# Kernel optimization log

Measured on AMD Instinct MI355X. Metric: run time of the kernel, lower is better.

## Reference

```python
import jax, jax.numpy as jnp
import numpy as np

B, Q, DIN, DOUT = 1, 1024, 4096, 4096
H, G, HD = 32, 8, 128          # heads, kv groups, head_dim; group_size = H // G
PREV = 3072                     # cached KV length
MAXPOS = 4096                   # rope table length (>= PREV + Q)
START = PREV


def _rope_tables(max_pos, head_dim):
    half = head_dim // 2
    inv_freq = 1.0 / (10000.0 ** (jnp.arange(half, dtype=jnp.float32) / half))
    ang = jnp.arange(max_pos, dtype=jnp.float32)[:, None] * inv_freq[None, :]
    ang = jnp.concatenate([ang, ang], axis=-1)  # [max_pos, head_dim]
    return jnp.cos(ang), jnp.sin(ang)


def apply_rope(x, cos, sin, start_pos):
    # x: [b, h, s, d]; rotate-half RoPE with absolute positions start_pos..start_pos+s
    s, d = x.shape[2], x.shape[3]
    c = cos[start_pos:start_pos + s]  # [s, d] (start_pos is a Python int)
    sn = sin[start_pos:start_pos + s]
    x1, x2 = x[..., : d // 2], x[..., d // 2:]
    rotated = jnp.concatenate([-x2, x1], axis=-1)
    return x * c + rotated * sn


def setup_inputs() -> dict:
    key = jax.random.key(0)
    ks = jax.random.split(key, 7)
    x = jax.random.normal(ks[0], (B, Q, DIN), dtype=jnp.float32)
    cos, sin = _rope_tables(MAXPOS, HD)
    # causal mask: query at abs position START+i may attend kv position j <= START+i
    qpos = START + jnp.arange(Q)
    kpos = jnp.arange(START + Q)
    mask = (kpos[None, :] > qpos[:, None])[None, None]  # [1,1,Q,KV], True = masked
    prev_k = jax.random.normal(ks[1], (B, G, PREV, HD), dtype=jnp.float32)
    prev_v = jax.random.normal(ks[2], (B, G, PREV, HD), dtype=jnp.float32)
    sc = 0.02
    Wq = jax.random.normal(ks[3], (DIN, DOUT), dtype=jnp.float32) * sc
    Wk = jax.random.normal(ks[4], (DIN, G * HD), dtype=jnp.float32) * sc
    Wv = jax.random.normal(ks[5], (DIN, G * HD), dtype=jnp.float32) * sc
    Wo = jax.random.normal(ks[6], (DOUT, DOUT), dtype=jnp.float32) * sc
    return dict(x=x, mask=mask, cos=cos, sin=sin, start_pos=START,
                prev_k=prev_k, prev_v=prev_v, Wq=Wq, Wk=Wk, Wv=Wv, Wo=Wo)


def reference(x, mask, cos, sin, start_pos, prev_k, prev_v, Wq, Wk, Wv, Wo):
    b, s, _ = x.shape
    gs = H // G  # group_size
    q = (x @ Wq).reshape(b, s, H, HD).transpose(0, 2, 1, 3)   # [b,H,s,hd]
    k = (x @ Wk).reshape(b, s, G, HD).transpose(0, 2, 1, 3)   # [b,G,s,hd]
    v = (x @ Wv).reshape(b, s, G, HD).transpose(0, 2, 1, 3)
    q = apply_rope(q, cos, sin, start_pos)
    k = apply_rope(k, cos, sin, start_pos)
    keys = jnp.concatenate([prev_k, k], axis=2)    # [b,G,KV,hd]
    values = jnp.concatenate([prev_v, v], axis=2)
    # grouped attention (equivalent to repeat_interleave of K/V over group_size)
    qg = q.reshape(b, G, gs, s, HD)
    scores = jnp.einsum('bgnqd,bgkd->bgnqk', qg, keys)        # [b,G,gs,s,KV]
    scores = jnp.where(mask[:, :, None], -jnp.inf, scores)
    attn = jax.nn.softmax(scores / np.sqrt(HD).astype(np.float32), axis=-1)
    ctx = jnp.einsum('bgnqk,bgkd->bgnqd', attn, values)       # [b,G,gs,s,hd]
    ctx = ctx.reshape(b, H, s, HD).transpose(0, 2, 1, 3).reshape(b, s, DOUT)
    out = ctx @ Wo
    return (out, keys, values)
```

## Files before the change

kernel.cpp:

```cpp
#include <hip/hip_runtime.h>

typedef unsigned short u16;
typedef unsigned int u32;
typedef __attribute__((ext_vector_type(4))) float f32x4;
typedef __attribute__((ext_vector_type(16))) float f32x16;
typedef __attribute__((ext_vector_type(8))) __bf16 bf16x8;
typedef __attribute__((ext_vector_type(4))) u16 u16x4;
typedef __attribute__((ext_vector_type(8))) u16 u16x8;
typedef __attribute__((ext_vector_type(4))) u32 u32x4;

#define START_POS 3072
#define NKV 4096
#define HD_ 128
#define SEQ 1024
#define DIN_ 4096
#define DQKV 6144

__device__ __forceinline__ void gll16(const void* g, void* l) {
  __builtin_amdgcn_global_load_lds((const __attribute__((address_space(1))) u32*)g,
                                   (__attribute__((address_space(3))) u32*)l, 16, 0, 0);
}
__device__ __forceinline__ u16 f2bf(float f) {
  u32 u = __builtin_bit_cast(u32, f);
  return (u16)((u + 0x7fffu + ((u >> 16) & 1u)) >> 16);
}
__device__ __forceinline__ u32 pack2bf(float a, float b) {
  return (u32)f2bf(a) | ((u32)f2bf(b) << 16);
}
__device__ __forceinline__ f32x4 mfma16(bf16x8 a, bf16x8 b, f32x4 c) {
  return __builtin_amdgcn_mfma_f32_16x16x32_bf16(a, b, c, 0, 0, 0);
}
__device__ __forceinline__ f32x16 mfma32(bf16x8 a, bf16x8 b, f32x16 c) {
  return __builtin_amdgcn_mfma_f32_32x32x16_bf16(a, b, c, 0, 0, 0);
}

__global__ __launch_bounds__(256) void wtrans(const float* __restrict__ W,
    u16* __restrict__ Wt, int N, int ntn, int row_off)
{
  __shared__ float T[64][68];
  int bid = blockIdx.x;
  int nt = bid % ntn, kt = bid / ntn;
  int t = threadIdx.x;
  int kl = t >> 4, nl4 = (t & 15) << 2;
#pragma unroll
  for (int r = 0; r < 4; r++) {
    int row = r * 16 + kl;
    f32x4 v = *(const f32x4*)(W + (size_t)(kt * 64 + row) * N + nt * 64 + nl4);
    T[row][nl4] = v[0]; T[row][nl4 + 1] = v[1]; T[row][nl4 + 2] = v[2]; T[row][nl4 + 3] = v[3];
  }
  __syncthreads();
  int nl = t >> 2, k0 = (t & 3) << 4;
  u16x8 lo, hi;
#pragma unroll
  for (int j = 0; j < 8; j++) lo[j] = f2bf(T[k0 + j][nl]);
#pragma unroll
  for (int j = 0; j < 8; j++) hi[j] = f2bf(T[k0 + 8 + j][nl]);
  u16* dst = Wt + (size_t)(row_off + nt * 64 + nl) * 4096 + kt * 64 + k0;
  *(u16x8*)dst = lo;
  *(u16x8*)(dst + 8) = hi;
}

__global__ __launch_bounds__(256) void cvt_bf16(const float* __restrict__ src,
    u16* __restrict__ dst, int n4)
{
  int i = blockIdx.x * 256 + threadIdx.x;
  if (i >= n4) return;
  f32x4 v = *(const f32x4*)(src + (size_t)i * 4);
  u16x4 o;
#pragma unroll
  for (int j = 0; j < 4; j++) o[j] = f2bf(v[j]);
  *(u16x4*)(dst + (size_t)i * 4) = o;
}

__global__ __launch_bounds__(256) void gemm_bt(
    const u16* __restrict__ A, const u16* __restrict__ Bt,
    float* __restrict__ C, int N, int K, int nbx)
{
  __shared__ u16 As[128 * 32];
  __shared__ u16 Bs[64 * 32];
  int nwg = (int)gridDim.x;
  int orig = blockIdx.x;
  int q8 = nwg >> 3, r8 = nwg & 7;
  int xcd = orig & 7, jj = orig >> 3;
  int wgid = (xcd < r8 ? xcd * (q8 + 1) : r8 * (q8 + 1) + (xcd - r8) * q8) + jj;
  int by = wgid / nbx, bx = wgid % nbx;
  int tid = threadIdx.x, lane = tid & 63, wid = tid >> 6;
  int wr = wid >> 1, wc = wid & 1;
  int c = lane & 15, hh = lane >> 4;
  int lrow = wid * 16 + (lane >> 2);
  int ksl = (lane & 3) << 3;
  const u16* aS0 = A + (size_t)(by * 128 + lrow) * K + ksl;
  const u16* bS0 = Bt + (size_t)(bx * 64 + lrow) * K + ksl;
  u16* aL0 = As + wid * 512;
  u16* bL0 = Bs + wid * 512;
  f32x4 acc[4][2] = {};
  for (int k0 = 0; k0 < K; k0 += 32) {
    gll16(aS0 + k0, aL0);
    gll16(aS0 + (size_t)64 * K + k0, aL0 + 2048);
    gll16(bS0 + k0, bL0);
    __syncthreads();
    bf16x8 af[4], bf[2];
#pragma unroll
    for (int i = 0; i < 4; i++)
      af[i] = *(const bf16x8*)(As + (wr * 64 + i * 16 + c) * 32 + hh * 8);
#pragma unroll
    for (int i = 0; i < 2; i++)
      bf[i] = *(const bf16x8*)(Bs + (wc * 32 + i * 16 + c) * 32 + hh * 8);
#pragma unroll
    for (int mi = 0; mi < 4; mi++)
#pragma unroll
      for (int ni = 0; ni < 2; ni++)
        acc[mi][ni] = mfma16(af[mi], bf[ni], acc[mi][ni]);
    __syncthreads();
  }
  int row0 = by * 128 + wr * 64 + hh * 4;
  int col0 = bx * 64 + wc * 32 + c;
#pragma unroll
  for (int mi = 0; mi < 4; mi++)
#pragma unroll
    for (int ni = 0; ni < 2; ni++)
#pragma unroll
      for (int i = 0; i < 4; i++)
        C[(size_t)(row0 + mi * 16 + i) * N + col0 + ni * 16] = acc[mi][ni][i];
}

__global__ __launch_bounds__(256) void rope_q(const float* __restrict__ qkv,
    const float* __restrict__ cosb, const float* __restrict__ sinb, u16* __restrict__ qb)
{
  int tid = blockIdx.x * 256 + threadIdx.x;
  int dq = tid & 15, h = (tid >> 4) & 31, s = tid >> 9;
  int d = dq << 2;
  const float* base = qkv + (size_t)s * DQKV + h * HD_ + d;
  f32x4 a = *(const f32x4*)base;
  f32x4 b2 = *(const f32x4*)(base + 64);
  f32x4 cc = *(const f32x4*)(cosb + (size_t)(START_POS + s) * HD_ + d);
  f32x4 sn = *(const f32x4*)(sinb + (size_t)(START_POS + s) * HD_ + d);
  u16x4 o1, o2;
#pragma unroll
  for (int i = 0; i < 4; i++) {
    o1[i] = f2bf(a[i] * cc[i] - b2[i] * sn[i]);
    o2[i] = f2bf(b2[i] * cc[i] + a[i] * sn[i]);
  }
  u16* dst = qb + ((size_t)h * SEQ + s) * HD_ + d;
  *(u16x4*)dst = o1;
  *(u16x4*)(dst + 64) = o2;
}

__global__ __launch_bounds__(256) void rope_k(const float* __restrict__ qkv,
    const float* __restrict__ cosb, const float* __restrict__ sinb,
    float* __restrict__ keys, u16* __restrict__ kbb)
{
  int tid = blockIdx.x * 256 + threadIdx.x;
  int dq = tid & 15, g = (tid >> 4) & 7, s = tid >> 7;
  int d = dq << 2;
  const float* base = qkv + (size_t)s * DQKV + DIN_ + g * HD_ + d;
  f32x4 a = *(const f32x4*)base;
  f32x4 b2 = *(const f32x4*)(base + 64);
  f32x4 cc = *(const f32x4*)(cosb + (size_t)(START_POS + s) * HD_ + d);
  f32x4 sn = *(const f32x4*)(sinb + (size_t)(START_POS + s) * HD_ + d);
  f32x4 o1, o2;
  u16x4 p1, p2;
#pragma unroll
  for (int i = 0; i < 4; i++) {
    o1[i] = a[i] * cc[i] - b2[i] * sn[i];
    o2[i] = b2[i] * cc[i] + a[i] * sn[i];
    p1[i] = f2bf(o1[i]);
    p2[i] = f2bf(o2[i]);
  }
  size_t off = ((size_t)g * NKV + START_POS + s) * HD_ + d;
  *(f32x4*)(keys + off) = o1;
  *(f32x4*)(keys + off + 64) = o2;
  *(u16x4*)(kbb + off) = p1;
  *(u16x4*)(kbb + off + 64) = p2;
}

__global__ __launch_bounds__(256) void copy_vnew(const float* __restrict__ qkv,
    float* __restrict__ values)
{
  int tid = blockIdx.x * 256 + threadIdx.x;
  int dq = tid & 31, g = (tid >> 5) & 7, s = tid >> 8;
  int d = dq << 2;
  f32x4 v = *(const f32x4*)(qkv + (size_t)s * DQKV + DIN_ + 1024 + g * HD_ + d);
  *(f32x4*)(values + ((size_t)g * NKV + START_POS + s) * HD_ + d) = v;
}

__global__ __launch_bounds__(256) void prev_copy(const float* __restrict__ pk,
    const float* __restrict__ pv, float* __restrict__ keys, float* __restrict__ values,
    u16* __restrict__ kbb)
{
  int idx = blockIdx.x * 256 + threadIdx.x;
  int d4 = idx & 31;
  int rest = idx >> 5;
  int p = rest % 3072, g = rest / 3072;
  f32x4 kq = *(const f32x4*)(pk + (size_t)idx * 4);
  f32x4 vq = *(const f32x4*)(pv + (size_t)idx * 4);
  size_t off = ((size_t)g * NKV + p) * HD_ + d4 * 4;
  *(f32x4*)(keys + off) = kq;
  *(f32x4*)(values + off) = vq;
  u16x4 kb4;
#pragma unroll
  for (int i = 0; i < 4; i++) kb4[i] = f2bf(kq[i]);
  *(u16x4*)(kbb + off) = kb4;
}

__global__ __launch_bounds__(256) void vtrans(const float* __restrict__ pv,
    const float* __restrict__ qkv, u16* __restrict__ vT)
{
  __shared__ float T[64][68];
  int bid = blockIdx.x;
  int dt = bid & 1, pt = (bid >> 1) & 63, g = bid >> 7;
  int t = threadIdx.x;
  int pl = t >> 4, dl4 = (t & 15) << 2;
#pragma unroll
  for (int r = 0; r < 4; r++) {
    int row = r * 16 + pl;
    int pos = pt * 64 + row;
    f32x4 v;
    if (pos < START_POS)
      v = *(const f32x4*)(pv + ((size_t)g * START_POS + pos) * HD_ + dt * 64 + dl4);
    else
      v = *(const f32x4*)(qkv + (size_t)(pos - START_POS) * DQKV + 5120 + g * HD_ + dt * 64 + dl4);
    T[row][dl4] = v[0]; T[row][dl4 + 1] = v[1]; T[row][dl4 + 2] = v[2]; T[row][dl4 + 3] = v[3];
  }
  __syncthreads();
  int dl = t >> 2, p0 = (t & 3) << 4;
  u16x8 lo, hi;
#pragma unroll
  for (int j = 0; j < 8; j++) lo[j] = f2bf(T[p0 + j][dl]);
#pragma unroll
  for (int j = 0; j < 8; j++) hi[j] = f2bf(T[p0 + 8 + j][dl]);
  u16* dst = vT + ((size_t)g * HD_ + dt * 64 + dl) * NKV + pt * 64 + p0;
  *(u16x8*)dst = lo;
  *(u16x8*)(dst + 8) = hi;
}

__global__ __launch_bounds__(128, 2) void attn_fwd(
    const u16* __restrict__ qb, const u16* __restrict__ kb,
    const u16* __restrict__ vT, float* __restrict__ Opart, float* __restrict__ Ml)
{
  __shared__ u16 Ks[2 * 32 * 128];
  __shared__ u16 Vs[2 * 128 * 32];
  const float C2 = 0.12751744f;
  int bid = blockIdx.x;
  int g = bid & 7, j = bid >> 3;
  int sp = j >> 6, jj = j & 63;
  int h = g * 4 + (jj >> 4), qt = jj & 15;
  int tid = threadIdx.x, lane = tid & 63, w = tid >> 6;
  int c32 = lane & 31, h8 = lane >> 5;
  int qw0 = qt * 64 + w * 32;
  bf16x8 Qf[8];
#pragma unroll
  for (int dc = 0; dc < 8; dc++)
    Qf[dc] = *(const bf16x8*)(qb + ((size_t)(h * 1024 + qw0 + c32)) * 128 + dc * 16 + h8 * 8);
  f32x16 O0 = {}, O1 = {}, O2 = {}, O3 = {};
  float Mx = -1e30f, Ls = 0.f;
  int t0 = sp ? (49 + qt) : 0;
  int t1 = sp ? (98 + 2 * qt) : (49 + qt);

#define STAGE_KV(tt, bo) do { \
  _Pragma("unroll") \
  for (int r = 0; r < 4; r++) { \
    int s = w * 256 + r * 64 + lane; \
    int krow = s >> 4, sl = s & 15; \
    gll16(kb + ((size_t)(g * 4096 + (tt) * 32 + krow)) * 128 + (sl ^ (krow & 7)) * 8, \
          Ks + (bo) + (w * 256 + r * 64) * 8); \
    int d = s >> 2, sl2 = s & 3; \
    gll16(vT + ((size_t)(g * 128 + d)) * 4096 + (tt) * 32 + (sl2 ^ ((d >> 1) & 3)) * 8, \
          Vs + (bo) + (w * 256 + r * 64) * 8); \
  } \
} while (0)

  int cur = 0;
  STAGE_KV(t0, 0);
  __syncthreads();
  int vxr = (c32 >> 1) & 3;
  for (int t = t0; t < t1; t++) {
    if (t + 1 < t1) STAGE_KV(t + 1, (cur ^ 1) * 4096);
    const u16* Kb = Ks + cur * 4096;
    const u16* Vb = Vs + cur * 4096;
    f32x16 S0 = {};
#pragma unroll
    for (int dc = 0; dc < 8; dc++) {
      int sx = (2 * dc + h8) ^ (c32 & 7);
      bf16x8 k0 = *(const bf16x8*)(Kb + (size_t)c32 * 128 + sx * 8);
      S0 = mfma32(k0, Qf[dc], S0);
    }
    if (t * 32 + 31 > START_POS + qw0) {
      int qa = START_POS + qw0 + c32;
#pragma unroll
      for (int r = 0; r < 16; r++) {
        int kvo = t * 32 + (r & 3) + 8 * (r >> 2) + 4 * h8;
        if (kvo > qa) S0[r] = -1e30f;
      }
    }
    float tm[16];
#pragma unroll
    for (int r = 0; r < 16; r++) tm[r] = S0[r];
#pragma unroll
    for (int sft = 8; sft >= 1; sft >>= 1)
#pragma unroll
      for (int r = 0; r < sft; r++) tm[r] = fmaxf(tm[r], tm[r + sft]);
    float full = fmaxf(tm[0], __shfl_xor(tm[0], 32));
    if (!__all(full <= Mx + 62.0f)) {
      float Mn = fmaxf(Mx, full);
      float al = exp2f((Mx - Mn) * C2);
      Mx = Mn;
      Ls *= al;
#pragma unroll
      for (int r = 0; r < 16; r++) { O0[r] *= al; O1[r] *= al; O2[r] *= al; O3[r] *= al; }
    }
#pragma unroll
    for (int r = 0; r < 16; r++) S0[r] = exp2f((S0[r] - Mx) * C2);
    float ts[16];
#pragma unroll
    for (int r = 0; r < 16; r++) ts[r] = S0[r];
#pragma unroll
    for (int sft = 8; sft >= 1; sft >>= 1)
#pragma unroll
      for (int r = 0; r < sft; r++) ts[r] = ts[r] + ts[r + sft];
    Ls += ts[0] + __shfl_xor(ts[0], 32);
    u32 pk0[8], x0[8];
#pragma unroll
    for (int m = 0; m < 8; m++) pk0[m] = pack2bf(S0[2 * m], S0[2 * m + 1]);
#pragma unroll
    for (int m = 0; m < 8; m++) x0[m] = __shfl_xor(pk0[m], 32);
    bf16x8 pbf[2];
    {
      u32x4 f0 = { h8 ? x0[2] : pk0[0], h8 ? x0[3] : pk0[1],
                   h8 ? pk0[2] : x0[0], h8 ? pk0[3] : x0[1] };
      u32x4 f1 = { h8 ? x0[6] : pk0[4], h8 ? x0[7] : pk0[5],
                   h8 ? pk0[6] : x0[4], h8 ? pk0[7] : x0[5] };
      pbf[0] = __builtin_bit_cast(bf16x8, f0);
      pbf[1] = __builtin_bit_cast(bf16x8, f1);
    }
#pragma unroll
    for (int kc = 0; kc < 2; kc++) {
      int sv = 2 * kc + h8;
      int sx = (sv ^ vxr) * 8;
      {
        bf16x8 vf = *(const bf16x8*)(Vb + (size_t)(0 * 32 + c32) * 32 + sx);
        O0 = mfma32(vf, pbf[kc], O0);
      }
      {
        bf16x8 vf = *(const bf16x8*)(Vb + (size_t)(1 * 32 + c32) * 32 + sx);
        O1 = mfma32(vf, pbf[kc], O1);
      }
      {
        bf16x8 vf = *(const bf16x8*)(Vb + (size_t)(2 * 32 + c32) * 32 + sx);
        O2 = mfma32(vf, pbf[kc], O2);
      }
      {
        bf16x8 vf = *(const bf16x8*)(Vb + (size_t)(3 * 32 + c32) * 32 + sx);
        O3 = mfma32(vf, pbf[kc], O3);
      }
    }
    __syncthreads();
    cur ^= 1;
  }
#undef STAGE_KV
  {
    float* Orow = Opart + (size_t)sp * 4194304 + (size_t)(qw0 + c32) * 4096 + h * 128;
#pragma unroll
    for (int a = 0; a < 4; a++) {
      f32x4 o0, o1, o2, o3;
#pragma unroll
      for (int b = 0; b < 4; b++) {
        o0[b] = O0[4 * a + b]; o1[b] = O1[4 * a + b];
        o2[b] = O2[4 * a + b]; o3[b] = O3[4 * a + b];
      }
      int d0 = 8 * a + 4 * h8;
      *(f32x4*)(Orow + d0) = o0;
      *(f32x4*)(Orow + 32 + d0) = o1;
      *(f32x4*)(Orow + 64 + d0) = o2;
      *(f32x4*)(Orow + 96 + d0) = o3;
    }
    if (h8 == 0) {
      float* mp = Ml + ((size_t)(sp * 32 + h) * 1024 + qw0 + c32) * 2;
      mp[0] = Mx; mp[1] = Ls;
    }
  }
}

__global__ __launch_bounds__(256) void attn_combine(const float* __restrict__ Opart,
    const float* __restrict__ Ml, u16* __restrict__ ctxb)
{
  int idx = blockIdx.x * 256 + threadIdx.x;
  int q = idx >> 10, c4 = idx & 1023;
  int col = c4 * 4, h = col >> 7;
  const float* m0p = Ml + ((size_t)h * 1024 + q) * 2;
  const float* m1p = Ml + ((size_t)(32 + h) * 1024 + q) * 2;
  float m0 = m0p[0], l0 = m0p[1];
  float m1 = m1p[0], l1 = m1p[1];
  float M = fmaxf(m0, m1);
  float w0 = exp2f((m0 - M) * 0.12751744f);
  float w1 = exp2f((m1 - M) * 0.12751744f);
  float inv = 1.0f / (l0 * w0 + l1 * w1);
  f32x4 a = *(const f32x4*)(Opart + (size_t)q * 4096 + col);
  f32x4 b = *(const f32x4*)(Opart + 4194304 + (size_t)q * 4096 + col);
  u16x4 o;
#pragma unroll
  for (int i = 0; i < 4; i++) o[i] = f2bf((a[i] * w0 + b[i] * w1) * inv);
  *(u16x4*)(ctxb + (size_t)q * 4096 + col) = o;
}

extern "C" void kernel_launch(void* const* d_in, const int* in_sizes, int n_in,
                              void* d_out, int out_size, void* d_ws, size_t ws_size,
                              hipStream_t stream) {
  const float* x      = (const float*)d_in[0];
  const float* cosb   = (const float*)d_in[2];
  const float* sinb   = (const float*)d_in[3];
  const float* prev_k = (const float*)d_in[5];
  const float* prev_v = (const float*)d_in[6];
  const float* Wq     = (const float*)d_in[7];
  const float* Wk     = (const float*)d_in[8];
  const float* Wv     = (const float*)d_in[9];
  const float* Wo     = (const float*)d_in[10];

  u16* Wt_proj = (u16*)d_ws;
  u16* Wt_out  = Wt_proj + (size_t)6144 * 4096;
  u16* xb      = Wt_out + (size_t)4096 * 4096;
  float* qkv   = (float*)(xb + (size_t)1024 * 4096);
  u16* qb      = (u16*)(qkv + (size_t)1024 * 6144);
  u16* kbb     = qb + (size_t)32 * 1024 * 128;
  u16* vT      = kbb + (size_t)8 * 4096 * 128;
  u16* ctxb    = vT + (size_t)8 * 4096 * 128;
  float* Opart = (float*)d_ws;
  float* Ml    = Opart + (size_t)2 * 1024 * 4096;

  float* outp   = (float*)d_out;
  float* keys   = outp + (size_t)4194304;
  float* values = outp + (size_t)8388608;

  wtrans<<<4096, 256, 0, stream>>>(Wq, Wt_proj, 4096, 64, 0);
  wtrans<<<1024, 256, 0, stream>>>(Wk, Wt_proj, 1024, 16, 4096);
  wtrans<<<1024, 256, 0, stream>>>(Wv, Wt_proj, 1024, 16, 5120);
  wtrans<<<4096, 256, 0, stream>>>(Wo, Wt_out, 4096, 64, 0);
  cvt_bf16<<<4096, 256, 0, stream>>>(x, xb, 1048576);

  gemm_bt<<<768, 256, 0, stream>>>(xb, Wt_proj, qkv, 6144, 4096, 96);

  rope_q<<<2048, 256, 0, stream>>>(qkv, cosb, sinb, qb);
  rope_k<<<512, 256, 0, stream>>>(qkv, cosb, sinb, keys, kbb);
  copy_vnew<<<1024, 256, 0, stream>>>(qkv, values);
  prev_copy<<<3072, 256, 0, stream>>>(prev_k, prev_v, keys, values, kbb);
  vtrans<<<1024, 256, 0, stream>>>(prev_v, qkv, vT);

  attn_fwd<<<1024, 128, 0, stream>>>(qb, kbb, vT, Opart, Ml);
  attn_combine<<<4096, 256, 0, stream>>>(Opart, Ml, ctxb);

  gemm_bt<<<512, 256, 0, stream>>>(ctxb, Wt_out, outp, 4096, 4096, 64);
}
```

Measured before the change: 401.9 us.

## Use single-wave attention blocks with V fragments loaded directly into registers

The attention kernel now runs one 64-lane wave per block (2048 blocks) covering 32 queries. K tiles stay double-buffered in LDS via async global-to-LDS loads, while V fragments are read straight from global memory into registers. Block-wide barriers are replaced by explicit waitcnt and a sched_barrier, and the causal split point is recomputed per 32-query chunk. The bf16 packing also switches to the HIP intrinsic conversion. The aim is to drop barrier overhead and LDS traffic for V, at the cost of uncoalesced-ish global V loads and more register pressure, and the hand-tuned vmcnt counts are fragile.

```diff
diff --git a/kernel.cpp b/kernel.cpp
--- a/kernel.cpp
+++ b/kernel.cpp
@@ -1,4 +1,5 @@
 #include <hip/hip_runtime.h>
+#include <hip/hip_bf16.h>
 
 typedef unsigned short u16;
 typedef unsigned int u32;
@@ -25,7 +26,9 @@
   return (u16)((u + 0x7fffu + ((u >> 16) & 1u)) >> 16);
 }
 __device__ __forceinline__ u32 pack2bf(float a, float b) {
-  return (u32)f2bf(a) | ((u32)f2bf(b) << 16);
+  __hip_bfloat162 t = __float22bfloat162_rn(float2{a, b});
+  u32 u; __builtin_memcpy(&u, &t, 4);
+  return u;
 }
 __device__ __forceinline__ f32x4 mfma16(bf16x8 a, bf16x8 b, f32x4 c) {
   return __builtin_amdgcn_mfma_f32_16x16x32_bf16(a, b, c, 0, 0, 0);
@@ -234,50 +237,59 @@
   *(u16x8*)(dst + 8) = hi;
 }
 
-__global__ __launch_bounds__(128, 2) void attn_fwd(
+__global__ __launch_bounds__(64, 2) void attn_fwd(
     const u16* __restrict__ qb, const u16* __restrict__ kb,
     const u16* __restrict__ vT, float* __restrict__ Opart, float* __restrict__ Ml)
 {
   __shared__ u16 Ks[2 * 32 * 128];
-  __shared__ u16 Vs[2 * 128 * 32];
   const float C2 = 0.12751744f;
   int bid = blockIdx.x;
-  int g = bid & 7, j = bid >> 3;
-  int sp = j >> 6, jj = j & 63;
-  int h = g * 4 + (jj >> 4), qt = jj & 15;
-  int tid = threadIdx.x, lane = tid & 63, w = tid >> 6;
+  int g = bid & 7, r_ = bid >> 3;
+  int sp = r_ >> 7, rr = r_ & 127;
+  int h = g * 4 + (rr >> 5), qc = rr & 31;
+  int lane = threadIdx.x;
   int c32 = lane & 31, h8 = lane >> 5;
-  int qw0 = qt * 64 + w * 32;
+  int qw0 = qc * 32;
   bf16x8 Qf[8];
 #pragma unroll
   for (int dc = 0; dc < 8; dc++)
     Qf[dc] = *(const bf16x8*)(qb + ((size_t)(h * 1024 + qw0 + c32)) * 128 + dc * 16 + h8 * 8);
   f32x16 O0 = {}, O1 = {}, O2 = {}, O3 = {};
   float Mx = -1e30f, Ls = 0.f;
-  int t0 = sp ? (49 + qt) : 0;
-  int t1 = sp ? (98 + 2 * qt) : (49 + qt);
-
-#define STAGE_KV(tt, bo) do { \
+  int ntt = 97 + qc;
+  int th = (98 + qc) >> 1;
+  int t0 = sp ? th : 0;
+  int t1 = sp ? ntt : th;
+
+#define STAGE_K(tt, bo) do { \
   _Pragma("unroll") \
-  for (int r = 0; r < 4; r++) { \
-    int s = w * 256 + r * 64 + lane; \
+  for (int r = 0; r < 8; r++) { \
+    int s = r * 64 + lane; \
     int krow = s >> 4, sl = s & 15; \
     gll16(kb + ((size_t)(g * 4096 + (tt) * 32 + krow)) * 128 + (sl ^ (krow & 7)) * 8, \
-          Ks + (bo) + (w * 256 + r * 64) * 8); \
-    int d = s >> 2, sl2 = s & 3; \
-    gll16(vT + ((size_t)(g * 128 + d)) * 4096 + (tt) * 32 + (sl2 ^ ((d >> 1) & 3)) * 8, \
-          Vs + (bo) + (w * 256 + r * 64) * 8); \
+          Ks + (bo) + r * 512); \
   } \
 } while (0)
 
   int cur = 0;
-  STAGE_KV(t0, 0);
-  __syncthreads();
-  int vxr = (c32 >> 1) & 3;
+  STAGE_K(t0, 0);
   for (int t = t0; t < t1; t++) {
-    if (t + 1 < t1) STAGE_KV(t + 1, (cur ^ 1) * 4096);
+    asm volatile("s_waitcnt lgkmcnt(0)" ::: "memory");
+    bf16x8 vr[4][2];
+#pragma unroll
+    for (int db = 0; db < 4; db++)
+#pragma unroll
+      for (int kc = 0; kc < 2; kc++)
+        vr[db][kc] = *(const bf16x8*)(vT + ((size_t)(g * 128 + db * 32 + c32)) * 4096
+                                      + t * 32 + kc * 16 + h8 * 8);
+    if (t + 1 < t1) {
+      STAGE_K(t + 1, (cur ^ 1) * 4096);
+      asm volatile("s_waitcnt vmcnt(16)" ::: "memory");
+    } else {
+      asm volatile("s_waitcnt vmcnt(8)" ::: "memory");
+    }
+    __builtin_amdgcn_sched_barrier(0);
     const u16* Kb = Ks + cur * 4096;
-    const u16* Vb = Vs + cur * 4096;
     f32x16 S0 = {};
 #pragma unroll
     for (int dc = 0; dc < 8; dc++) {
@@ -335,29 +347,14 @@
     }
 #pragma unroll
     for (int kc = 0; kc < 2; kc++) {
-      int sv = 2 * kc + h8;
-      int sx = (sv ^ vxr) * 8;
-      {
-        bf16x8 vf = *(const bf16x8*)(Vb + (size_t)(0 * 32 + c32) * 32 + sx);
-        O0 = mfma32(vf, pbf[kc], O0);
-      }
-      {
-        bf16x8 vf = *(const bf16x8*)(Vb + (size_t)(1 * 32 + c32) * 32 + sx);
-        O1 = mfma32(vf, pbf[kc], O1);
-      }
-      {
-        bf16x8 vf = *(const bf16x8*)(Vb + (size_t)(2 * 32 + c32) * 32 + sx);
-        O2 = mfma32(vf, pbf[kc], O2);
-      }
-      {
-        bf16x8 vf = *(const bf16x8*)(Vb + (size_t)(3 * 32 + c32) * 32 + sx);
-        O3 = mfma32(vf, pbf[kc], O3);
-      }
-    }
-    __syncthreads();
+      O0 = mfma32(vr[0][kc], pbf[kc], O0);
+      O1 = mfma32(vr[1][kc], pbf[kc], O1);
+      O2 = mfma32(vr[2][kc], pbf[kc], O2);
+      O3 = mfma32(vr[3][kc], pbf[kc], O3);
+    }
     cur ^= 1;
   }
-#undef STAGE_KV
+#undef STAGE_K
   {
     float* Orow = Opart + (size_t)sp * 4194304 + (size_t)(qw0 + c32) * 4096 + h * 128;
 #pragma unroll
@@ -445,7 +442,7 @@
   prev_copy<<<3072, 256, 0, stream>>>(prev_k, prev_v, keys, values, kbb);
   vtrans<<<1024, 256, 0, stream>>>(prev_v, qkv, vT);
 
-  attn_fwd<<<1024, 128, 0, stream>>>(qb, kbb, vT, Opart, Ml);
+  attn_fwd<<<2048, 64, 0, stream>>>(qb, kbb, vT, Opart, Ml);
   attn_combine<<<4096, 256, 0, stream>>>(Opart, Ml, ctxb);
 
   gemm_bt<<<512, 256, 0, stream>>>(ctxb, Wt_out, outp, 4096, 4096, 64);
```

After: 439.2 us. 1.09x slower.
